# Performance work log

Hardware: AMD Instinct MI355X
Metric: run time of the kernel (lower is better)

## Reference

```python
import jax, jax.numpy as jnp
import numpy as np

B, T, N, D, H = 16, 96, 325, 64, 64
BS = 1e-09  # bias init constant

def _xavier(key, shape):
    fan_in, fan_out = shape
    limit = float(np.sqrt(6.0 / (fan_in + fan_out)))
    return jax.random.uniform(key, shape, jnp.float32, -limit, limit)

def setup_inputs() -> dict:
    key = jax.random.key(0)
    k = jax.random.split(key, 6)
    return {
        "x": jax.random.normal(k[0], (B, T, N, D), jnp.float32),
        "o_s": jax.random.normal(k[1], (B, T, N, D), jnp.float32),
        "U_x": _xavier(k[2], (D, 4 * H)),
        "V_x": _xavier(k[3], (H, 4 * H)),
        "b_x": jnp.full((4 * H,), BS, jnp.float32),
        "U_g": _xavier(k[4], (D, 2 * H)),
        "V_g": _xavier(k[5], (H, 2 * H)),
        "b_g": jnp.full((2 * H,), BS, jnp.float32),
    }

def reference(x, o_s, U_x, V_x, b_x, U_g, V_g, b_g):
    b, t, n, d = x.shape
    h = V_x.shape[0]
    ht0 = jnp.zeros((b, n, h), x.dtype)
    ct0 = jnp.zeros((b, n, h), x.dtype)

    def step(carry, inp):
        ht, ct = carry
        xt, ost = inp  # [b, n, d] each
        gates = xt @ U_x + ht @ V_x + b_x          # [b, n, 4h]
        gov = jax.nn.sigmoid(ost @ U_g + ht @ V_g + b_g)  # [b, n, 2h]
        ft = jax.nn.sigmoid(gates[..., :h])
        it = jax.nn.sigmoid(gates[..., h:2 * h])
        ot = jax.nn.sigmoid(gates[..., 2 * h:3 * h])
        ut = jax.nn.sigmoid(gates[..., 3 * h:])
        gov_f = gov[..., :h]
        gov_u = gov[..., h:]
        ct = gov_f * ft * ct + gov_u * it * ut
        ht = ot * jnp.tanh(ct)
        return (ht, ct), ht

    xs = (jnp.swapaxes(x, 0, 1), jnp.swapaxes(o_s, 0, 1))  # time-major [t, b, n, d]
    (ht, ct), hseq = jax.lax.scan(step, (ht0, ct0), xs)
    hidden_seq = jnp.swapaxes(hseq, 0, 1)  # [b, t, n, h]
    return hidden_seq, ht, ct
```

## Files before the change

### kernel.cpp

```cpp
#include <hip/hip_runtime.h>
#include <stdint.h>


#define TT 96
#define NNROW 325
#define STEP_OFS 20800
#define HT_OFS 31948800
#define CT_OFS 32281600

typedef __attribute__((ext_vector_type(8))) short short8;
typedef __attribute__((ext_vector_type(4))) float f32x4;

#define BAR() asm volatile("s_waitcnt lgkmcnt(0)\n\ts_barrier" ::: "memory")

__device__ __forceinline__ short f2bf(float f) {
    union { float f; uint32_t u; } v; v.f = f;
    uint32_t r = (v.u + 0x7FFFu + ((v.u >> 16) & 1u)) >> 16;
    return (short)(r & 0xFFFFu);
}
__device__ __forceinline__ float frcp(float x) { return __builtin_amdgcn_rcpf(x); }
__device__ __forceinline__ float ex2(float x)  { return __builtin_amdgcn_exp2f(x); }
__device__ __forceinline__ uint32_t cvtpk(float lo, float hi) {
    uint32_t r;
    asm("v_cvt_pk_bf16_f32 %0, %1, %2" : "=v"(r) : "v"(lo), "v"(hi));
    return r;
}

__global__ __launch_bounds__(512, 1)
void glstm_kernel(const float* __restrict__ x,
                  const float* __restrict__ o_s,
                  const float* __restrict__ U_x,
                  const float* __restrict__ V_x,
                  const float* __restrict__ b_x,
                  const float* __restrict__ U_g,
                  const float* __restrict__ V_g,
                  const float* __restrict__ b_g,
                  float* __restrict__ out)
{
    __shared__ __align__(16) short Xb[2][2][1024];
    __shared__ __align__(16) short Ob[2][2][1024];
    __shared__ __align__(16) short Hb[2][2][1024];

    const int tid  = threadIdx.x;
    const int half = tid >> 8;
    const int t8   = tid & 255;
    int g = blockIdx.x * 2 + half;
    if (g > NNROW - 1) g = NNROW - 1;
    const int lane = tid & 63;
    const int w    = (t8 >> 6);
    const int q    = lane >> 4;
    const int ln   = lane & 15;

    short8 fWx[4][2], fWh[4][2], fGo[2][2], fGh[2][2];
    #pragma unroll
    for (int gt = 0; gt < 4; ++gt) {
        const int col = gt * 64 + w * 16 + ln;
        #pragma unroll
        for (int kb = 0; kb < 2; ++kb) {
            short8 a, b;
            #pragma unroll
            for (int j = 0; j < 8; ++j) {
                const int row = kb * 32 + q * 8 + j;
                a[j] = f2bf(U_x[(size_t)row * 256 + col]);
                b[j] = f2bf(V_x[(size_t)row * 256 + col]);
            }
            fWx[gt][kb] = a; fWh[gt][kb] = b;
        }
    }
    #pragma unroll
    for (int gt = 0; gt < 2; ++gt) {
        const int col = gt * 64 + w * 16 + ln;
        #pragma unroll
        for (int kb = 0; kb < 2; ++kb) {
            short8 a, b;
            #pragma unroll
            for (int j = 0; j < 8; ++j) {
                const int row = kb * 32 + q * 8 + j;
                a[j] = f2bf(U_g[(size_t)row * 128 + col]);
                b[j] = f2bf(V_g[(size_t)row * 128 + col]);
            }
            fGo[gt][kb] = a; fGh[gt][kb] = b;
        }
    }

    const int sm = t8 >> 4;
    const int sd = t8 & 15;
    const int srow = g * 16 + sm;
    const int sb = srow / NNROW;
    const int sn = srow - sb * NNROW;
    const size_t sbase = ((size_t)(sb * TT) * NNROW + sn) * 64 + sd * 4;
    const int stofs = (sm * 64 + (((sd >> 1) ^ (sm & 7)) << 3) + (sd & 1) * 4) * 2;

    const int o0 = ln * 128 + (((q    ) ^ (ln & 7)) << 4);
    const int o1 = ln * 128 + (((4 + q) ^ (ln & 7)) << 4);

    const int ch = w * 16 + ln;
    const float NL2E = -1.44269504f;
    const float nbf  = NL2E * b_x[ch];
    const float nbi  = NL2E * b_x[64  + ch];
    const float nbo  = NL2E * b_x[128 + ch];
    const float nbu  = NL2E * b_x[192 + ch];
    const float nbgf = NL2E * b_g[ch];
    const float nbgu = NL2E * b_g[64 + ch];

    size_t obase[4];
    int    fo[4];
    int    hofs[4];
    #pragma unroll
    for (int e = 0; e < 4; ++e) {
        const int m = q * 4 + e;
        const int row = g * 16 + m;
        const int b = row / NNROW;
        const int n = row - b * NNROW;
        obase[e] = ((size_t)(b * TT) * NNROW + n) * 64 + ch;
        fo[e]    = (b * NNROW + n) * 64 + ch;
        hofs[e]  = m * 64 + ((((ch >> 3) ^ (m & 7)) << 3) | (ch & 7));
    }
    float ct4[4] = {0.f, 0.f, 0.f, 0.f};

    short* const Xh = &Xb[half][0][0];
    short* const Oh = &Ob[half][0][0];
    short* const Hh = &Hb[half][0][0];

    {
        float4 x0 = *(const float4*)(x   + sbase);
        float4 s0 = *(const float4*)(o_s + sbase);
        uint2 sx; sx.x = cvtpk(x0.x, x0.y); sx.y = cvtpk(x0.z, x0.w);
        uint2 so; so.x = cvtpk(s0.x, s0.y); so.y = cvtpk(s0.z, s0.w);
        *(uint2*)((char*)Xh + stofs) = sx;
        *(uint2*)((char*)Oh + stofs) = so;
        uint2 z; z.x = 0u; z.y = 0u;
        *(uint2*)((char*)Hh + t8 * 8) = z;
    }
    float4 xqA = *(const float4*)(x   + sbase + 1 * (size_t)STEP_OFS);
    float4 oqA = *(const float4*)(o_s + sbase + 1 * (size_t)STEP_OFS);
    float4 xqB = *(const float4*)(x   + sbase + 2 * (size_t)STEP_OFS);
    float4 oqB = *(const float4*)(o_s + sbase + 2 * (size_t)STEP_OFS);
    BAR();

    auto step = [&](int t, float4& xq, float4& oq) {
        const int p  = t & 1;
        const int pn = p ^ 1;
        const char* xb = (const char*)Xh + p * 2048;
        const char* ob = (const char*)Oh + p * 2048;
        const char* hb = (const char*)Hh + p * 2048;
        const short8 ax0 = *(const short8*)(xb + o0);
        const short8 ax1 = *(const short8*)(xb + o1);
        const short8 ao0 = *(const short8*)(ob + o0);
        const short8 ao1 = *(const short8*)(ob + o1);
        const short8 ah0 = *(const short8*)(hb + o0);
        const short8 ah1 = *(const short8*)(hb + o1);

        f32x4 aF[4], aG[2];
        #pragma unroll
        for (int gt = 0; gt < 4; ++gt) {
            f32x4 acc = {0.f, 0.f, 0.f, 0.f};
            acc = __builtin_amdgcn_mfma_f32_16x16x32_bf16(ax0, fWx[gt][0], acc, 0, 0, 0);
            acc = __builtin_amdgcn_mfma_f32_16x16x32_bf16(ax1, fWx[gt][1], acc, 0, 0, 0);
            acc = __builtin_amdgcn_mfma_f32_16x16x32_bf16(ah0, fWh[gt][0], acc, 0, 0, 0);
            acc = __builtin_amdgcn_mfma_f32_16x16x32_bf16(ah1, fWh[gt][1], acc, 0, 0, 0);
            aF[gt] = acc;
        }
        #pragma unroll
        for (int gt = 0; gt < 2; ++gt) {
            f32x4 acc = {0.f, 0.f, 0.f, 0.f};
            acc = __builtin_amdgcn_mfma_f32_16x16x32_bf16(ao0, fGo[gt][0], acc, 0, 0, 0);
            acc = __builtin_amdgcn_mfma_f32_16x16x32_bf16(ao1, fGo[gt][1], acc, 0, 0, 0);
            acc = __builtin_amdgcn_mfma_f32_16x16x32_bf16(ah0, fGh[gt][0], acc, 0, 0, 0);
            acc = __builtin_amdgcn_mfma_f32_16x16x32_bf16(ah1, fGh[gt][1], acc, 0, 0, 0);
            aG[gt] = acc;
        }

        {
            uint2 sx; sx.x = cvtpk(xq.x, xq.y); sx.y = cvtpk(xq.z, xq.w);
            uint2 so; so.x = cvtpk(oq.x, oq.y); so.y = cvtpk(oq.z, oq.w);
            *(uint2*)((char*)Xh + pn * 2048 + stofs) = sx;
            *(uint2*)((char*)Oh + pn * 2048 + stofs) = so;
            int tn = t + 3; if (tn > TT - 1) tn = TT - 1;
            xq = *(const float4*)(x   + sbase + (size_t)tn * STEP_OFS);
            oq = *(const float4*)(o_s + sbase + (size_t)tn * STEP_OFS);
        }

        const size_t tofs = (size_t)t * STEP_OFS;
        float hv[4];
        #pragma unroll
        for (int e = 0; e < 4; ++e) {
            float ef  = ex2(fmaf(aF[0][e], NL2E, nbf));
            float ei  = ex2(fmaf(aF[1][e], NL2E, nbi));
            float eo  = ex2(fmaf(aF[2][e], NL2E, nbo));
            float eu  = ex2(fmaf(aF[3][e], NL2E, nbu));
            float egf = ex2(fmaf(aG[0][e], NL2E, nbgf));
            float egu = ex2(fmaf(aG[1][e], NL2E, nbgu));
            float rf = frcp((1.f + ef) * (1.f + egf));
            float ru = frcp(((1.f + ei) * (1.f + eu)) * (1.f + egu));
            float c  = fmaf(ct4[e], rf, ru);
            ct4[e] = c;
            float E  = ex2(c * 2.88539008f);
            float th = fmaf(-2.f, frcp(E + 1.f), 1.f);
            float h  = th * frcp(1.f + eo);
            hv[e] = h;
            out[obase[e] + tofs] = h;
            if (t == TT - 1) {
                out[HT_OFS + fo[e]] = h;
                out[CT_OFS + fo[e]] = c;
            }
        }

        {
            union { uint32_t u; short s[2]; } h01, h23;
            h01.u = cvtpk(hv[0], hv[1]);
            h23.u = cvtpk(hv[2], hv[3]);
            short* hn = (short*)((char*)Hh + pn * 2048);
            hn[hofs[0]] = h01.s[0];
            hn[hofs[1]] = h01.s[1];
            hn[hofs[2]] = h23.s[0];
            hn[hofs[3]] = h23.s[1];
        }
        BAR();
    };

    for (int t = 0; t < TT; t += 2) {
        step(t,     xqA, oqA);
        step(t + 1, xqB, oqB);
    }
}

extern "C" void kernel_launch(void* const* d_in, const int* in_sizes, int n_in,
                              void* d_out, int out_size, void* d_ws, size_t ws_size,
                              hipStream_t stream) {
    const float* x   = (const float*)d_in[0];
    const float* o_s = (const float*)d_in[1];
    const float* U_x = (const float*)d_in[2];
    const float* V_x = (const float*)d_in[3];
    const float* b_x = (const float*)d_in[4];
    const float* U_g = (const float*)d_in[5];
    const float* V_g = (const float*)d_in[6];
    const float* b_g = (const float*)d_in[7];
    float* out = (float*)d_out;

    glstm_kernel<<<dim3(163), dim3(512), 0, stream>>>(x, o_s, U_x, V_x, b_x, U_g, V_g, b_g, out);
}
```

Measured before the change: 344.2 us.

## Precompute next-step input projections off the recurrent critical path and merge reciprocals

```diff
diff --git a/kernel.cpp b/kernel.cpp
--- a/kernel.cpp
+++ b/kernel.cpp
@@ -47,7 +47,7 @@
     int g = blockIdx.x * 2 + half;
     if (g > NNROW - 1) g = NNROW - 1;
     const int lane = tid & 63;
-    const int w    = (t8 >> 6);
+    const int w    = t8 >> 6;
     const int q    = lane >> 4;
     const int ln   = lane & 15;
 
@@ -103,16 +103,14 @@
     const float nbgf = NL2E * b_g[ch];
     const float nbgu = NL2E * b_g[64 + ch];
 
-    size_t obase[4];
-    int    fo[4];
-    int    hofs[4];
+    int obase[4], fo[4], hofs[4];
     #pragma unroll
     for (int e = 0; e < 4; ++e) {
         const int m = q * 4 + e;
         const int row = g * 16 + m;
         const int b = row / NNROW;
         const int n = row - b * NNROW;
-        obase[e] = ((size_t)(b * TT) * NNROW + n) * 64 + ch;
+        obase[e] = ((b * TT) * NNROW + n) * 64 + ch;
         fo[e]    = (b * NNROW + n) * 64 + ch;
         hofs[e]  = m * 64 + ((((ch >> 3) ^ (m & 7)) << 3) | (ch & 7));
     }
@@ -125,63 +123,99 @@
     {
         float4 x0 = *(const float4*)(x   + sbase);
         float4 s0 = *(const float4*)(o_s + sbase);
-        uint2 sx; sx.x = cvtpk(x0.x, x0.y); sx.y = cvtpk(x0.z, x0.w);
-        uint2 so; so.x = cvtpk(s0.x, s0.y); so.y = cvtpk(s0.z, s0.w);
-        *(uint2*)((char*)Xh + stofs) = sx;
-        *(uint2*)((char*)Oh + stofs) = so;
+        float4 x1 = *(const float4*)(x   + sbase + (size_t)STEP_OFS);
+        float4 s1 = *(const float4*)(o_s + sbase + (size_t)STEP_OFS);
+        uint2 v;
+        v.x = cvtpk(x0.x, x0.y); v.y = cvtpk(x0.z, x0.w);
+        *(uint2*)((char*)Xh + stofs) = v;
+        v.x = cvtpk(s0.x, s0.y); v.y = cvtpk(s0.z, s0.w);
+        *(uint2*)((char*)Oh + stofs) = v;
+        v.x = cvtpk(x1.x, x1.y); v.y = cvtpk(x1.z, x1.w);
+        *(uint2*)((char*)Xh + 2048 + stofs) = v;
+        v.x = cvtpk(s1.x, s1.y); v.y = cvtpk(s1.z, s1.w);
+        *(uint2*)((char*)Oh + 2048 + stofs) = v;
         uint2 z; z.x = 0u; z.y = 0u;
         *(uint2*)((char*)Hh + t8 * 8) = z;
     }
-    float4 xqA = *(const float4*)(x   + sbase + 1 * (size_t)STEP_OFS);
-    float4 oqA = *(const float4*)(o_s + sbase + 1 * (size_t)STEP_OFS);
-    float4 xqB = *(const float4*)(x   + sbase + 2 * (size_t)STEP_OFS);
-    float4 oqB = *(const float4*)(o_s + sbase + 2 * (size_t)STEP_OFS);
+    float4 xqA = *(const float4*)(x   + sbase + 2 * (size_t)STEP_OFS);
+    float4 oqA = *(const float4*)(o_s + sbase + 2 * (size_t)STEP_OFS);
+    float4 xqB = *(const float4*)(x   + sbase + 3 * (size_t)STEP_OFS);
+    float4 oqB = *(const float4*)(o_s + sbase + 3 * (size_t)STEP_OFS);
     BAR();
 
-    auto step = [&](int t, float4& xq, float4& oq) {
-        const int p  = t & 1;
-        const int pn = p ^ 1;
-        const char* xb = (const char*)Xh + p * 2048;
-        const char* ob = (const char*)Oh + p * 2048;
-        const char* hb = (const char*)Hh + p * 2048;
+    f32x4 xF[4], xG[2];
+    {
+        const char* xb = (const char*)Xh;
+        const char* ob = (const char*)Oh;
         const short8 ax0 = *(const short8*)(xb + o0);
         const short8 ax1 = *(const short8*)(xb + o1);
         const short8 ao0 = *(const short8*)(ob + o0);
         const short8 ao1 = *(const short8*)(ob + o1);
+        const f32x4 z = {0.f, 0.f, 0.f, 0.f};
+        #pragma unroll
+        for (int gt = 0; gt < 4; ++gt) {
+            f32x4 a = __builtin_amdgcn_mfma_f32_16x16x32_bf16(ax0, fWx[gt][0], z, 0, 0, 0);
+            xF[gt]  = __builtin_amdgcn_mfma_f32_16x16x32_bf16(ax1, fWx[gt][1], a, 0, 0, 0);
+        }
+        #pragma unroll
+        for (int gt = 0; gt < 2; ++gt) {
+            f32x4 a = __builtin_amdgcn_mfma_f32_16x16x32_bf16(ao0, fGo[gt][0], z, 0, 0, 0);
+            xG[gt]  = __builtin_amdgcn_mfma_f32_16x16x32_bf16(ao1, fGo[gt][1], a, 0, 0, 0);
+        }
+    }
+    BAR();
+
+    auto step = [&](int t, float4& xq, float4& oq) {
+        const int p  = t & 1;
+        const int pn = p ^ 1;
+
+        const char* hb = (const char*)Hh + p * 2048;
         const short8 ah0 = *(const short8*)(hb + o0);
         const short8 ah1 = *(const short8*)(hb + o1);
+        const char* xbn = (const char*)Xh + pn * 2048;
+        const char* obn = (const char*)Oh + pn * 2048;
+        const short8 ax0 = *(const short8*)(xbn + o0);
+        const short8 ax1 = *(const short8*)(xbn + o1);
+        const short8 ao0 = *(const short8*)(obn + o0);
+        const short8 ao1 = *(const short8*)(obn + o1);
 
         f32x4 aF[4], aG[2];
         #pragma unroll
         for (int gt = 0; gt < 4; ++gt) {
-            f32x4 acc = {0.f, 0.f, 0.f, 0.f};
-            acc = __builtin_amdgcn_mfma_f32_16x16x32_bf16(ax0, fWx[gt][0], acc, 0, 0, 0);
-            acc = __builtin_amdgcn_mfma_f32_16x16x32_bf16(ax1, fWx[gt][1], acc, 0, 0, 0);
-            acc = __builtin_amdgcn_mfma_f32_16x16x32_bf16(ah0, fWh[gt][0], acc, 0, 0, 0);
-            acc = __builtin_amdgcn_mfma_f32_16x16x32_bf16(ah1, fWh[gt][1], acc, 0, 0, 0);
-            aF[gt] = acc;
+            f32x4 a = __builtin_amdgcn_mfma_f32_16x16x32_bf16(ah0, fWh[gt][0], xF[gt], 0, 0, 0);
+            aF[gt]  = __builtin_amdgcn_mfma_f32_16x16x32_bf16(ah1, fWh[gt][1], a, 0, 0, 0);
         }
         #pragma unroll
         for (int gt = 0; gt < 2; ++gt) {
-            f32x4 acc = {0.f, 0.f, 0.f, 0.f};
-            acc = __builtin_amdgcn_mfma_f32_16x16x32_bf16(ao0, fGo[gt][0], acc, 0, 0, 0);
-            acc = __builtin_amdgcn_mfma_f32_16x16x32_bf16(ao1, fGo[gt][1], acc, 0, 0, 0);
-            acc = __builtin_amdgcn_mfma_f32_16x16x32_bf16(ah0, fGh[gt][0], acc, 0, 0, 0);
-            acc = __builtin_amdgcn_mfma_f32_16x16x32_bf16(ah1, fGh[gt][1], acc, 0, 0, 0);
-            aG[gt] = acc;
+            f32x4 a = __builtin_amdgcn_mfma_f32_16x16x32_bf16(ah0, fGh[gt][0], xG[gt], 0, 0, 0);
+            aG[gt]  = __builtin_amdgcn_mfma_f32_16x16x32_bf16(ah1, fGh[gt][1], a, 0, 0, 0);
+        }
+
+        {
+            const f32x4 z = {0.f, 0.f, 0.f, 0.f};
+            #pragma unroll
+            for (int gt = 0; gt < 4; ++gt) {
+                f32x4 a = __builtin_amdgcn_mfma_f32_16x16x32_bf16(ax0, fWx[gt][0], z, 0, 0, 0);
+                xF[gt]  = __builtin_amdgcn_mfma_f32_16x16x32_bf16(ax1, fWx[gt][1], a, 0, 0, 0);
+            }
+            #pragma unroll
+            for (int gt = 0; gt < 2; ++gt) {
+                f32x4 a = __builtin_amdgcn_mfma_f32_16x16x32_bf16(ao0, fGo[gt][0], z, 0, 0, 0);
+                xG[gt]  = __builtin_amdgcn_mfma_f32_16x16x32_bf16(ao1, fGo[gt][1], a, 0, 0, 0);
+            }
         }
 
         {
             uint2 sx; sx.x = cvtpk(xq.x, xq.y); sx.y = cvtpk(xq.z, xq.w);
             uint2 so; so.x = cvtpk(oq.x, oq.y); so.y = cvtpk(oq.z, oq.w);
-            *(uint2*)((char*)Xh + pn * 2048 + stofs) = sx;
-            *(uint2*)((char*)Oh + pn * 2048 + stofs) = so;
-            int tn = t + 3; if (tn > TT - 1) tn = TT - 1;
+            *(uint2*)((char*)Xh + p * 2048 + stofs) = sx;
+            *(uint2*)((char*)Oh + p * 2048 + stofs) = so;
+            int tn = t + 4; if (tn > TT - 1) tn = TT - 1;
             xq = *(const float4*)(x   + sbase + (size_t)tn * STEP_OFS);
             oq = *(const float4*)(o_s + sbase + (size_t)tn * STEP_OFS);
         }
 
-        const size_t tofs = (size_t)t * STEP_OFS;
+        const int tofs = t * STEP_OFS;
         float hv[4];
         #pragma unroll
         for (int e = 0; e < 4; ++e) {
@@ -191,13 +225,12 @@
             float eu  = ex2(fmaf(aF[3][e], NL2E, nbu));
             float egf = ex2(fmaf(aG[0][e], NL2E, nbgf));
             float egu = ex2(fmaf(aG[1][e], NL2E, nbgu));
-            float rf = frcp((1.f + ef) * (1.f + egf));
-            float ru = frcp(((1.f + ei) * (1.f + eu)) * (1.f + egu));
-            float c  = fmaf(ct4[e], rf, ru);
+            float P1 = (1.f + ef) * (1.f + egf);
+            float P2 = (1.f + ei) * (1.f + eu) * (1.f + egu);
+            float c  = fmaf(ct4[e], P2, P1) * frcp(P1 * P2);
             ct4[e] = c;
-            float E  = ex2(c * 2.88539008f);
-            float th = fmaf(-2.f, frcp(E + 1.f), 1.f);
-            float h  = th * frcp(1.f + eo);
+            float E  = ex2(fminf(c * 2.88539008f, 60.f));
+            float h  = (E - 1.f) * frcp((E + 1.f) * (1.f + eo));
             hv[e] = h;
             out[obase[e] + tofs] = h;
             if (t == TT - 1) {
```

Result: no change. 340.8 us (-1.0%).
